# Kernel optimization log

Measured on AMD Instinct MI355X. Metric: run time of the kernel, lower is better.

The kernel has to match this reference:

```python
import jax, jax.numpy as jnp
import numpy as np
import math

D_MODEL = 1024
N_HEADS = 16
D_K = D_MODEL // N_HEADS
MAX_REL = 32


def setup_inputs() -> dict:
    key = jax.random.key(0)
    ks = jax.random.split(key, 8)
    B, S = 8, 1024
    x = jax.random.normal(ks[0], (B, S, D_MODEL), dtype=jnp.float32)
    scale = 1.0 / math.sqrt(D_MODEL)
    Wq = jax.random.normal(ks[1], (D_MODEL, D_MODEL), dtype=jnp.float32) * scale
    Wk = jax.random.normal(ks[2], (D_MODEL, D_MODEL), dtype=jnp.float32) * scale
    Wv = jax.random.normal(ks[3], (D_MODEL, D_MODEL), dtype=jnp.float32) * scale
    Wo = jax.random.normal(ks[4], (D_MODEL, D_MODEL), dtype=jnp.float32) * scale
    b_o = jnp.zeros((D_MODEL,), dtype=jnp.float32)
    rel_k_emb = jax.random.normal(ks[5], (2 * MAX_REL + 1, D_K), dtype=jnp.float32) * 0.02
    rel_v_emb = jax.random.normal(ks[6], (2 * MAX_REL + 1, D_K), dtype=jnp.float32) * 0.02
    return {"x": x, "Wq": Wq, "Wk": Wk, "Wv": Wv, "Wo": Wo, "b_o": b_o,
            "rel_k_emb": rel_k_emb, "rel_v_emb": rel_v_emb}


def reference(x, Wq, Wk, Wv, Wo, b_o, rel_k_emb, rel_v_emb):
    B, S, D = x.shape
    H, dk = N_HEADS, D_K
    inv_sqrt_dk = 1.0 / math.sqrt(dk)
    # projections (torch Linear: x @ W.T), split heads -> [B, S, H, dk]
    Q = (x @ Wq.T).reshape(B, S, H, dk)
    K = (x @ Wk.T).reshape(B, S, H, dk)
    V = (x @ Wv.T).reshape(B, S, H, dk)
    # relative position indices: clip(j - i, -M, M) + M  -> [S, S]
    pos = jnp.arange(S)
    rel_idx = jnp.clip(pos[None, :] - pos[:, None], -MAX_REL, MAX_REL) + MAX_REL
    rel_k = rel_k_emb[rel_idx]  # [S, S, dk]
    rel_v = rel_v_emb[rel_idx]  # [S, S, dk]
    # scores: content term + Shaw relative-key term, both scaled by 1/sqrt(dk)
    scores = jnp.einsum('bihd,bjhd->bhij', Q, K) * inv_sqrt_dk
    scores = scores + jnp.einsum('bihd,ijd->bhij', Q, rel_k) * inv_sqrt_dk
    attn = jax.nn.softmax(scores, axis=-1)  # [B, H, S, S]
    # context: attn @ V + Shaw relative-value term
    ctx = jnp.einsum('bhij,bjhd->bihd', attn, V)
    ctx = ctx + jnp.einsum('bhij,ijd->bihd', attn, rel_v)
    ctx = ctx.reshape(B, S, D)
    out = ctx @ Wo.T + b_o
    return out
```

## Files before the change

### kernel.cpp

```cpp
#include <hip/hip_runtime.h>
#include <hip/hip_bf16.h>
#include <stdint.h>

typedef __bf16 bf16;
typedef __bf16 bf16x8 __attribute__((ext_vector_type(8)));
typedef short s16x4 __attribute__((ext_vector_type(4)));
typedef float f32x4 __attribute__((ext_vector_type(4)));

#define DEVI __device__ __forceinline__

static constexpr int QREL_ST = 80;
static constexpr float SCL2 = 0.1803368801111244f;

DEVI void gload_lds16(const void* g, void* l) {
  __builtin_amdgcn_global_load_lds(
      (const __attribute__((address_space(1))) void*)g,
      (__attribute__((address_space(3))) void*)l, 16, 0, 0);
}

__global__ __launch_bounds__(256) void k_cvt(const float* __restrict__ s,
                                             bf16* __restrict__ d, int n4) {
  int i = blockIdx.x * 256 + threadIdx.x;
  if (i >= n4) return;
  float4 v = ((const float4*)s)[i];
  union { bf16 b[4]; ushort4 u; } pk;
  pk.b[0] = (bf16)v.x; pk.b[1] = (bf16)v.y;
  pk.b[2] = (bf16)v.z; pk.b[3] = (bf16)v.w;
  ((ushort4*)d)[i] = pk.u;
}

__global__ __launch_bounds__(256) void k_cvtw(const float* __restrict__ a,
                                              const float* __restrict__ b,
                                              const float* __restrict__ c,
                                              const float* __restrict__ e,
                                              bf16* __restrict__ d) {
  int z = blockIdx.y;
  const float* s = (z == 0) ? a : (z == 1) ? b : (z == 2) ? c : e;
  int i = blockIdx.x * 256 + threadIdx.x;
  float4 v = ((const float4*)s)[i];
  union { bf16 bb[4]; ushort4 u; } pk;
  pk.bb[0] = (bf16)v.x; pk.bb[1] = (bf16)v.y;
  pk.bb[2] = (bf16)v.z; pk.bb[3] = (bf16)v.w;
  ((ushort4*)(d + (size_t)z * 1048576))[i] = pk.u;
}

template <int MODE>
DEVI void gemm_core(const bf16* __restrict__ A, const bf16* __restrict__ W,
                    const float* __restrict__ bo, bf16* __restrict__ OutB,
                    float* __restrict__ OutF, int m0, int n0) {
  const int tid = threadIdx.x, wid = tid >> 6, lane = tid & 63;
  const int wr = wid >> 1, wc = wid & 1;
  __shared__ __attribute__((aligned(16))) bf16 As[128 * 32];
  __shared__ __attribute__((aligned(16))) bf16 Bs[128 * 32];
  f32x4 acc[4][4] = {};
  const int lrow = lane >> 2, lcol = (lane & 3) * 8;
  for (int k0 = 0; k0 < 1024; k0 += 32) {
    for (int c = wid; c < 8; c += 4) {
      gload_lds16(&A[(size_t)(m0 + c * 16 + lrow) * 1024 + k0 + lcol], &As[c * 512]);
      gload_lds16(&W[(size_t)(n0 + c * 16 + lrow) * 1024 + k0 + lcol], &Bs[c * 512]);
    }
    __syncthreads();
    bf16x8 af[4], bw[4];
#pragma unroll
    for (int f = 0; f < 4; ++f) {
      af[f] = *(const bf16x8*)&As[(wr * 64 + f * 16 + (lane & 15)) * 32 + (lane >> 4) * 8];
      bw[f] = *(const bf16x8*)&Bs[(wc * 64 + f * 16 + (lane & 15)) * 32 + (lane >> 4) * 8];
    }
#pragma unroll
    for (int fm = 0; fm < 4; ++fm)
#pragma unroll
      for (int fn = 0; fn < 4; ++fn)
        acc[fm][fn] = __builtin_amdgcn_mfma_f32_16x16x32_bf16(af[fm], bw[fn], acc[fm][fn], 0, 0, 0);
    __syncthreads();
  }
#pragma unroll
  for (int fm = 0; fm < 4; ++fm)
#pragma unroll
    for (int fn = 0; fn < 4; ++fn)
#pragma unroll
      for (int r = 0; r < 4; ++r) {
        int m = m0 + wr * 64 + fm * 16 + (lane >> 4) * 4 + r;
        int n = n0 + wc * 64 + fn * 16 + (lane & 15);
        if (MODE == 0) {
          size_t o = ((size_t)((m >> 10) * 16 + (n >> 6)) * 1024 + (m & 1023)) * 64 + (n & 63);
          OutB[o] = (bf16)acc[fm][fn][r];
        } else {
          OutF[(size_t)m * 1024 + n] = acc[fm][fn][r] + bo[n];
        }
      }
}

__global__ __launch_bounds__(256) void k_gemm_qkv(const bf16* __restrict__ A,
                                                  const bf16* __restrict__ Wb,
                                                  bf16* __restrict__ Qb,
                                                  bf16* __restrict__ Kb,
                                                  bf16* __restrict__ Vb) {
  const int z = blockIdx.z;
  const bf16* W = Wb + (size_t)z * 1024 * 1024;
  bf16* Out = (z == 0) ? Qb : ((z == 1) ? Kb : Vb);
  gemm_core<0>(A, W, nullptr, Out, nullptr, blockIdx.x * 128, blockIdx.y * 128);
}

__global__ __launch_bounds__(256) void k_gemm_out(const bf16* __restrict__ A,
                                                  const bf16* __restrict__ W,
                                                  const float* __restrict__ bo,
                                                  float* __restrict__ Out) {
  gemm_core<1>(A, W, bo, nullptr, Out, blockIdx.x * 128, blockIdx.y * 128);
}

__global__ __launch_bounds__(256) void k_transpose(const bf16* __restrict__ Vb,
                                                   bf16* __restrict__ Vt) {
  const int s0 = blockIdx.x * 64, bh = blockIdx.y;
  __shared__ __attribute__((aligned(16))) bf16 T[64 * 72];
  const int tid = threadIdx.x;
#pragma unroll
  for (int c = 0; c < 2; ++c) {
    int flat = c * 256 + tid;
    int row = flat >> 3, c8 = (flat & 7) * 8;
    *(uint4*)&T[row * 72 + c8] =
        *(const uint4*)&Vb[((size_t)bh * 1024 + s0 + row) * 64 + c8];
  }
  __syncthreads();
  const int d = tid >> 2, j0 = (tid & 3) * 16;
  union { bf16 b[16]; uint4 u[2]; } pk;
#pragma unroll
  for (int j = 0; j < 16; ++j) pk.b[j] = T[(j0 + j) * 72 + d];
  size_t base = ((size_t)bh * 64 + d) * 1024 + s0 + j0;
  *(uint4*)&Vt[base] = pk.u[0];
  *(uint4*)&Vt[base + 8] = pk.u[1];
}

__global__ __launch_bounds__(256) void k_qrel(const bf16* __restrict__ Qb,
                                              const float* __restrict__ relk,
                                              bf16* __restrict__ Qrel) {
  const int m0 = blockIdx.x * 64;
  const int tid = threadIdx.x, wid = tid >> 6, lane = tid & 63;
  __shared__ __attribute__((aligned(16))) bf16 RK[80 * 72];
  for (int i = tid; i < 80 * 72; i += 256) {
    int r = i / 72, dd = i % 72;
    RK[i] = (r < 65 && dd < 64) ? (bf16)relk[r * 64 + dd] : (bf16)0.0f;
  }
  __syncthreads();
  bf16x8 qa[2];
#pragma unroll
  for (int kk = 0; kk < 2; ++kk)
    qa[kk] = *(const bf16x8*)&Qb[(size_t)(m0 + wid * 16 + (lane & 15)) * 64 + kk * 32 + (lane >> 4) * 8];
  f32x4 acc[5] = {};
#pragma unroll
  for (int fc = 0; fc < 5; ++fc)
#pragma unroll
    for (int kk = 0; kk < 2; ++kk) {
      bf16x8 rb = *(const bf16x8*)&RK[(fc * 16 + (lane & 15)) * 72 + kk * 32 + (lane >> 4) * 8];
      acc[fc] = __builtin_amdgcn_mfma_f32_16x16x32_bf16(qa[kk], rb, acc[fc], 0, 0, 0);
    }
#pragma unroll
  for (int fc = 0; fc < 5; ++fc)
#pragma unroll
    for (int r = 0; r < 4; ++r)
      Qrel[(size_t)(m0 + wid * 16 + (lane >> 4) * 4 + r) * QREL_ST + fc * 16 + (lane & 15)] =
          (bf16)(acc[fc][r] * SCL2);
}

__global__ __launch_bounds__(256) void k_prep(const float* __restrict__ relv,
                                              bf16* __restrict__ RVt) {
  int i = blockIdx.x * 256 + threadIdx.x;
  if (i >= 64 * 96) return;
  int d = i / 96, r = i % 96;
  RVt[i] = (r < 65) ? (bf16)relv[r * 64 + d] : (bf16)0.0f;
}

__global__ __launch_bounds__(256, 4) void k_attn(const bf16* __restrict__ Qb,
                                                 const bf16* __restrict__ Kb,
                                                 const bf16* __restrict__ Vt,
                                                 const bf16* __restrict__ Qrel,
                                                 const bf16* __restrict__ RVt,
                                                 const float* __restrict__ relv,
                                                 bf16* __restrict__ Ctx) {
  const int jb = blockIdx.x;
  const int xcd = jb & 7, rlin = jb >> 3;
  const int bh = xcd + 8 * (rlin >> 4);
  const int tq = rlin & 15, q0 = tq * 64;
  const int tid = threadIdx.x, wid = tid >> 6, lane = tid & 63;
  __shared__ __attribute__((aligned(16))) bf16 Qrl[64 * 72];
  __shared__ __attribute__((aligned(16))) bf16 KS[64 * 64];
  __shared__ __attribute__((aligned(16))) bf16 VS[64 * 64];
  __shared__ __attribute__((aligned(16))) bf16 BUK[64 * 64];

  for (int i = tid; i < 576; i += 256) {
    int row = i / 9, u4 = (i % 9) * 8;
    *(uint4*)&Qrl[row * 72 + u4] =
        *(const uint4*)&Qrel[((size_t)bh * 1024 + q0 + row) * QREL_ST + u4];
  }
  {
    uint4 z4 = {0, 0, 0, 0};
    uint4* bz = (uint4*)BUK;
    for (int i = tid; i < 512; i += 256) bz[i] = z4;
  }

  const int q16 = lane & 15, lhi = lane >> 4;
  const int qrow = wid * 16 + q16;
  const int qglob = q0 + qrow;
  const size_t kvb = (size_t)bh * 65536;

  const int srow = lane >> 3;
  const int scol = (((lane & 7) ^ srow)) * 8;

  const bf16* kg0 = Kb + kvb + (size_t)((wid * 2 + 0) * 8 + srow) * 64 + scol;
  const bf16* kg1 = Kb + kvb + (size_t)((wid * 2 + 1) * 8 + srow) * 64 + scol;
  const bf16* vg0 = Vt + kvb + (size_t)((wid * 2 + 0) * 8 + srow) * 1024 + scol;
  const bf16* vg1 = Vt + kvb + (size_t)((wid * 2 + 1) * 8 + srow) * 1024 + scol;
  bf16* kd0 = &KS[(wid * 2 + 0) * 512];
  bf16* kd1 = &KS[(wid * 2 + 1) * 512];
  bf16* vd0 = &VS[(wid * 2 + 0) * 512];
  bf16* vd1 = &VS[(wid * 2 + 1) * 512];

#define STAGE_ISSUE()                                                          \
  do {                                                                         \
    gload_lds16(kg0, kd0); gload_lds16(kg1, kd1);                              \
    gload_lds16(vg0, vd0); gload_lds16(vg1, vd1);                              \
    kg0 += 4096; kg1 += 4096; vg0 += 64; vg1 += 64;                            \
  } while (0)

  bf16x8 qa[2];
#pragma unroll
  for (int kk = 0; kk < 2; ++kk)
    qa[kk] = *(const bf16x8*)&Qb[kvb + (size_t)qglob * 64 + kk * 32 + lhi * 8];

  f32x4 o[4] = {};
  float rowsum = 0.f, sumL = 0.f, sumR = 0.f;

  union PU { bf16 b[4]; s16x4 s; };
  union VU { uint2 u; s16x4 s; };

  STAGE_ISSUE();
  __syncthreads();
  const float biasL = (float)Qrl[qrow * 72 + 0];
  const float biasR = (float)Qrl[qrow * 72 + 64];

  const int swz = (q16 & 7) * 8;
  const bf16* kp0 = &KS[q16 * 64 + ((lhi * 8) ^ swz)];
  const bf16* kp1 = &KS[q16 * 64 + ((32 + lhi * 8) ^ swz)];
  const bf16* vp[4] = {
      &VS[q16 * 64 + ((0 * 16 + lhi * 4) ^ swz)],
      &VS[q16 * 64 + ((1 * 16 + lhi * 4) ^ swz)],
      &VS[q16 * 64 + ((2 * 16 + lhi * 4) ^ swz)],
      &VS[q16 * 64 + ((3 * 16 + lhi * 4) ^ swz)]};
  const bf16* qrp = &Qrl[qrow * 72 + 32];
  bf16* bkp = &BUK[qrow * 64 + 32];

  for (int t = 0; t < 16; ++t) {
    const int kv0 = t * 64;
    const int kind = (t <= tq - 2) ? 0 : (t >= tq + 2) ? 1 : 2;
    f32x4 st[4] = {};
    __builtin_amdgcn_s_setprio(1);
#pragma unroll
    for (int jt = 0; jt < 4; ++jt) {
      bf16x8 k0 = *(const bf16x8*)(kp0 + jt * 1024);
      bf16x8 k1 = *(const bf16x8*)(kp1 + jt * 1024);
      st[jt] = __builtin_amdgcn_mfma_f32_16x16x32_bf16(k0, qa[0], st[jt], 0, 0, 0);
      st[jt] = __builtin_amdgcn_mfma_f32_16x16x32_bf16(k1, qa[1], st[jt], 0, 0, 0);
    }
    __builtin_amdgcn_s_setprio(0);
    PU pk[4];
    if (kind == 0) {
#pragma unroll
      for (int jt = 0; jt < 4; ++jt)
#pragma unroll
        for (int r = 0; r < 4; ++r) {
          float p = __builtin_amdgcn_exp2f(__builtin_fmaf(st[jt][r], SCL2, biasL));
          rowsum += p; sumL += p;
          pk[jt].b[r] = (bf16)p;
        }
    } else if (kind == 1) {
#pragma unroll
      for (int jt = 0; jt < 4; ++jt)
#pragma unroll
        for (int r = 0; r < 4; ++r) {
          float p = __builtin_amdgcn_exp2f(__builtin_fmaf(st[jt][r], SCL2, biasR));
          rowsum += p; sumR += p;
          pk[jt].b[r] = (bf16)p;
        }
    } else {
#pragma unroll
      for (int jt = 0; jt < 4; ++jt)
#pragma unroll
        for (int r = 0; r < 4; ++r) {
          const int j = kv0 + jt * 16 + lhi * 4 + r;
          const int delta = j - qglob;
          const int dc = delta < -32 ? -32 : (delta > 32 ? 32 : delta);
          const float b = (float)qrp[dc];
          float p = __builtin_amdgcn_exp2f(__builtin_fmaf(st[jt][r], SCL2, b));
          rowsum += p;
          pk[jt].b[r] = (bf16)p;
          if (delta <= -32) sumL += p;
          else if (delta >= 32) sumR += p;
          else bkp[delta] = (bf16)p;
        }
    }
    __builtin_amdgcn_s_setprio(1);
#pragma unroll
    for (int jt = 0; jt < 4; ++jt)
#pragma unroll
      for (int fd = 0; fd < 4; ++fd) {
        VU v;
        v.u = *(const uint2*)(vp[jt] + fd * 1024);
        o[fd] = __builtin_amdgcn_mfma_f32_16x16x16bf16_1k(pk[jt].s, v.s, o[fd], 0, 0, 0);
      }
    __builtin_amdgcn_s_setprio(0);
    __syncthreads();
    if (t < 15) {
      STAGE_ISSUE();
      __syncthreads();
    }
  }
#undef STAGE_ISSUE

  rowsum += __shfl_xor(rowsum, 16, 64);
  rowsum += __shfl_xor(rowsum, 32, 64);
  sumL += __shfl_xor(sumL, 16, 64);
  sumL += __shfl_xor(sumL, 32, 64);
  sumR += __shfl_xor(sumR, 16, 64);
  sumR += __shfl_xor(sumR, 32, 64);
  if (lhi == 0) BUK[qrow * 64 + 0] = (bf16)sumL;

  float linv[4], sumRr[4];
#pragma unroll
  for (int r = 0; r < 4; ++r) {
    linv[r] = 1.0f / __shfl(rowsum, lhi * 4 + r, 16);
    sumRr[r] = __shfl(sumR, lhi * 4 + r, 16);
  }

#pragma unroll
  for (int kk = 0; kk < 2; ++kk) {
    bf16x8 pa = *(const bf16x8*)&BUK[(wid * 16 + q16) * 64 + kk * 32 + lhi * 8];
#pragma unroll
    for (int fd = 0; fd < 4; ++fd) {
      bf16x8 rb = *(const bf16x8*)&RVt[(fd * 16 + q16) * 96 + kk * 32 + lhi * 8];
      o[fd] = __builtin_amdgcn_mfma_f32_16x16x32_bf16(pa, rb, o[fd], 0, 0, 0);
    }
  }
#pragma unroll
  for (int fd = 0; fd < 4; ++fd) {
    float rv64 = relv[64 * 64 + fd * 16 + q16];
#pragma unroll
    for (int r = 0; r < 4; ++r) o[fd][r] += sumRr[r] * rv64;
  }

  const int rbase = wid * 16 + lhi * 4;
  __syncthreads();
  bf16* OL = Qrl;
#pragma unroll
  for (int fd = 0; fd < 4; ++fd)
#pragma unroll
    for (int r = 0; r < 4; ++r)
      OL[(rbase + r) * 72 + fd * 16 + q16] = (bf16)(o[fd][r] * linv[r]);
  __syncthreads();
  {
    int il = tid >> 2, d0 = (tid & 3) * 16;
    union { bf16 b[16]; uint4 u[2]; } pkk;
#pragma unroll
    for (int c = 0; c < 16; ++c) pkk.b[c] = OL[il * 72 + d0 + c];
    size_t base = ((size_t)(bh >> 4) * 1024 + q0 + il) * 1024 + (bh & 15) * 64 + d0;
    *(uint4*)&Ctx[base] = pkk.u[0];
    *(uint4*)&Ctx[base + 8] = pkk.u[1];
  }
}

extern "C" void kernel_launch(void* const* d_in, const int* in_sizes, int n_in,
                              void* d_out, int out_size, void* d_ws, size_t ws_size,
                              hipStream_t stream) {
  const float* x = (const float*)d_in[0];
  const float* Wq = (const float*)d_in[1];
  const float* Wk = (const float*)d_in[2];
  const float* Wv = (const float*)d_in[3];
  const float* Wo = (const float*)d_in[4];
  const float* bo = (const float*)d_in[5];
  const float* relk = (const float*)d_in[6];
  const float* relv = (const float*)d_in[7];
  float* out = (float*)d_out;

  uint8_t* w = (uint8_t*)d_ws;
  bf16* xb = (bf16*)(w);
  bf16* Wb = (bf16*)(w + 16777216);
  bf16* Qb = (bf16*)(w + 25165824);
  bf16* Kb = (bf16*)(w + 41943040);
  bf16* Vb = (bf16*)(w + 58720256);
  bf16* Vt = (bf16*)(w + 75497472);
  bf16* Qrel = (bf16*)(w + 92274688);
  bf16* Ctx = Vb;
  bf16* RVt = xb;

  k_cvt<<<8192, 256, 0, stream>>>(x, xb, 2097152);
  k_cvtw<<<dim3(1024, 4), 256, 0, stream>>>(Wq, Wk, Wv, Wo, Wb);

  dim3 gg(64, 8, 3);
  k_gemm_qkv<<<gg, 256, 0, stream>>>(xb, Wb, Qb, Kb, Vb);
  k_transpose<<<dim3(16, 128), 256, 0, stream>>>(Vb, Vt);
  k_qrel<<<2048, 256, 0, stream>>>(Qb, relk, Qrel);
  k_prep<<<24, 256, 0, stream>>>(relv, RVt);
  k_attn<<<2048, 256, 0, stream>>>(Qb, Kb, Vt, Qrel, RVt, relv, Ctx);
  k_gemm_out<<<dim3(64, 8), 256, 0, stream>>>(Ctx, Wb + 3 * 1048576, bo, out);
}
```

Before: 199.7 us.

## Double-buffer K/V tiles in attention and XCD-remap GEMM block indices

The attention kernel now keeps two K/V LDS buffers and prefetches tile t+2 while computing tile t. It waits with explicit vmcnt counts and raw barriers instead of two syncthreads per iteration, which is meant to hide global-to-LDS latency. The LDS footprint grows, so occupancy is lowered to 3 blocks. The QKV and output GEMMs switch to a 1D grid whose block index is remapped so neighbouring tiles land on the same XCD, aiming at better L2 reuse.

```diff
diff --git a/kernel.cpp b/kernel.cpp
--- a/kernel.cpp
+++ b/kernel.cpp
@@ -95,17 +95,22 @@
                                                   bf16* __restrict__ Qb,
                                                   bf16* __restrict__ Kb,
                                                   bf16* __restrict__ Vb) {
-  const int z = blockIdx.z;
+  const int j = blockIdx.x;
+  const int l = (j & 7) * 192 + (j >> 3);
+  const int x = l & 63, y = (l >> 6) & 7, z = l >> 9;
   const bf16* W = Wb + (size_t)z * 1024 * 1024;
   bf16* Out = (z == 0) ? Qb : ((z == 1) ? Kb : Vb);
-  gemm_core<0>(A, W, nullptr, Out, nullptr, blockIdx.x * 128, blockIdx.y * 128);
+  gemm_core<0>(A, W, nullptr, Out, nullptr, x * 128, y * 128);
 }
 
 __global__ __launch_bounds__(256) void k_gemm_out(const bf16* __restrict__ A,
                                                   const bf16* __restrict__ W,
                                                   const float* __restrict__ bo,
                                                   float* __restrict__ Out) {
-  gemm_core<1>(A, W, bo, nullptr, Out, blockIdx.x * 128, blockIdx.y * 128);
+  const int j = blockIdx.x;
+  const int l = (j & 7) * 64 + (j >> 3);
+  const int x = l & 63, y = l >> 6;
+  gemm_core<1>(A, W, bo, nullptr, Out, x * 128, y * 128);
 }
 
 __global__ __launch_bounds__(256) void k_transpose(const bf16* __restrict__ Vb,
@@ -169,7 +174,7 @@
   RVt[i] = (r < 65) ? (bf16)relv[r * 64 + d] : (bf16)0.0f;
 }
 
-__global__ __launch_bounds__(256, 4) void k_attn(const bf16* __restrict__ Qb,
+__global__ __launch_bounds__(256, 3) void k_attn(const bf16* __restrict__ Qb,
                                                  const bf16* __restrict__ Kb,
                                                  const bf16* __restrict__ Vt,
                                                  const bf16* __restrict__ Qrel,
@@ -182,8 +187,8 @@
   const int tq = rlin & 15, q0 = tq * 64;
   const int tid = threadIdx.x, wid = tid >> 6, lane = tid & 63;
   __shared__ __attribute__((aligned(16))) bf16 Qrl[64 * 72];
-  __shared__ __attribute__((aligned(16))) bf16 KS[64 * 64];
-  __shared__ __attribute__((aligned(16))) bf16 VS[64 * 64];
+  __shared__ __attribute__((aligned(16))) bf16 KS[2 * 64 * 64];
+  __shared__ __attribute__((aligned(16))) bf16 VS[2 * 64 * 64];
   __shared__ __attribute__((aligned(16))) bf16 BUK[64 * 64];
 
   for (int i = tid; i < 576; i += 256) {
@@ -209,15 +214,13 @@
   const bf16* kg1 = Kb + kvb + (size_t)((wid * 2 + 1) * 8 + srow) * 64 + scol;
   const bf16* vg0 = Vt + kvb + (size_t)((wid * 2 + 0) * 8 + srow) * 1024 + scol;
   const bf16* vg1 = Vt + kvb + (size_t)((wid * 2 + 1) * 8 + srow) * 1024 + scol;
-  bf16* kd0 = &KS[(wid * 2 + 0) * 512];
-  bf16* kd1 = &KS[(wid * 2 + 1) * 512];
-  bf16* vd0 = &VS[(wid * 2 + 0) * 512];
-  bf16* vd1 = &VS[(wid * 2 + 1) * 512];
-
-#define STAGE_ISSUE()                                                          \
+  const int c0 = (wid * 2 + 0) * 512, c1 = (wid * 2 + 1) * 512;
+
+#define STAGE(T)                                                               \
   do {                                                                         \
-    gload_lds16(kg0, kd0); gload_lds16(kg1, kd1);                              \
-    gload_lds16(vg0, vd0); gload_lds16(vg1, vd1);                              \
+    const int b_ = ((T) & 1) * 4096;                                           \
+    gload_lds16(kg0, &KS[b_ + c0]); gload_lds16(kg1, &KS[b_ + c1]);            \
+    gload_lds16(vg0, &VS[b_ + c0]); gload_lds16(vg1, &VS[b_ + c1]);            \
     kg0 += 4096; kg1 += 4096; vg0 += 64; vg1 += 64;                            \
   } while (0)
 
@@ -232,7 +235,8 @@
   union PU { bf16 b[4]; s16x4 s; };
   union VU { uint2 u; s16x4 s; };
 
-  STAGE_ISSUE();
+  STAGE(0);
+  STAGE(1);
   __syncthreads();
   const float biasL = (float)Qrl[qrow * 72 + 0];
   const float biasR = (float)Qrl[qrow * 72 + 64];
@@ -249,14 +253,20 @@
   bf16* bkp = &BUK[qrow * 64 + 32];
 
   for (int t = 0; t < 16; ++t) {
+    if (t < 15) asm volatile("s_waitcnt vmcnt(4)" ::: "memory");
+    else        asm volatile("s_waitcnt vmcnt(0)" ::: "memory");
+    __builtin_amdgcn_s_barrier();
+    __builtin_amdgcn_sched_barrier(0);
+
     const int kv0 = t * 64;
+    const int boff = (t & 1) * 4096;
     const int kind = (t <= tq - 2) ? 0 : (t >= tq + 2) ? 1 : 2;
     f32x4 st[4] = {};
     __builtin_amdgcn_s_setprio(1);
 #pragma unroll
     for (int jt = 0; jt < 4; ++jt) {
-      bf16x8 k0 = *(const bf16x8*)(kp0 + jt * 1024);
-      bf16x8 k1 = *(const bf16x8*)(kp1 + jt * 1024);
+      bf16x8 k0 = *(const bf16x8*)(kp0 + boff + jt * 1024);
+      bf16x8 k1 = *(const bf16x8*)(kp1 + boff + jt * 1024);
       st[jt] = __builtin_amdgcn_mfma_f32_16x16x32_bf16(k0, qa[0], st[jt], 0, 0, 0);
       st[jt] = __builtin_amdgcn_mfma_f32_16x16x32_bf16(k1, qa[1], st[jt], 0, 0, 0);
     }
@@ -303,17 +313,15 @@
 #pragma unroll
       for (int fd = 0; fd < 4; ++fd) {
         VU v;
-        v.u = *(const uint2*)(vp[jt] + fd * 1024);
+        v.u = *(const uint2*)(vp[jt] + boff + fd * 1024);
         o[fd] = __builtin_amdgcn_mfma_f32_16x16x16bf16_1k(pk[jt].s, v.s, o[fd], 0, 0, 0);
       }
     __builtin_amdgcn_s_setprio(0);
-    __syncthreads();
-    if (t < 15) {
-      STAGE_ISSUE();
-      __syncthreads();
-    }
-  }
-#undef STAGE_ISSUE
+
+    __builtin_amdgcn_s_barrier();
+    if (t < 14) STAGE(t + 2);
+  }
+#undef STAGE
 
   rowsum += __shfl_xor(rowsum, 16, 64);
   rowsum += __shfl_xor(rowsum, 32, 64);
@@ -393,11 +401,10 @@
   k_cvt<<<8192, 256, 0, stream>>>(x, xb, 2097152);
   k_cvtw<<<dim3(1024, 4), 256, 0, stream>>>(Wq, Wk, Wv, Wo, Wb);
 
-  dim3 gg(64, 8, 3);
-  k_gemm_qkv<<<gg, 256, 0, stream>>>(xb, Wb, Qb, Kb, Vb);
+  k_gemm_qkv<<<1536, 256, 0, stream>>>(xb, Wb, Qb, Kb, Vb);
   k_transpose<<<dim3(16, 128), 256, 0, stream>>>(Vb, Vt);
   k_qrel<<<2048, 256, 0, stream>>>(Qb, relk, Qrel);
   k_prep<<<24, 256, 0, stream>>>(relv, RVt);
   k_attn<<<2048, 256, 0, stream>>>(Qb, Kb, Vt, Qrel, RVt, relv, Ctx);
-  k_gemm_out<<<dim3(64, 8), 256, 0, stream>>>(Ctx, Wb + 3 * 1048576, bo, out);
-}
+  k_gemm_out<<<512, 256, 0, stream>>>(Ctx, Wb + 3 * 1048576, bo, out);
+}
```

Result: slower. 220.4 us (+10.3%).

## Enlarge attention query tile to 128 rows with 512-thread blocks

Applied to the files above, without the earlier changes.

The attention kernel now handles 128 query rows per block with 8 waves instead of 64 rows with 4 waves, so each K/V tile loaded into LDS serves twice as many queries. Each wave issues half as many staged loads, and the near/far classification of each tile is now done per wave rather than per block. The cost is more LDS per block (larger Qrel and bucket buffers), half as many blocks, and a 512-thread barrier on every iteration, which may reduce occupancy and latency hiding.

```diff
diff --git a/kernel.cpp b/kernel.cpp
--- a/kernel.cpp
+++ b/kernel.cpp
@@ -169,7 +169,7 @@
   RVt[i] = (r < 65) ? (bf16)relv[r * 64 + d] : (bf16)0.0f;
 }
 
-__global__ __launch_bounds__(256, 4) void k_attn(const bf16* __restrict__ Qb,
+__global__ __launch_bounds__(512, 6) void k_attn(const bf16* __restrict__ Qb,
                                                  const bf16* __restrict__ Kb,
                                                  const bf16* __restrict__ Vt,
                                                  const bf16* __restrict__ Qrel,
@@ -178,15 +178,15 @@
                                                  bf16* __restrict__ Ctx) {
   const int jb = blockIdx.x;
   const int xcd = jb & 7, rlin = jb >> 3;
-  const int bh = xcd + 8 * (rlin >> 4);
-  const int tq = rlin & 15, q0 = tq * 64;
+  const int bh = xcd + 8 * (rlin >> 3);
+  const int q0 = (rlin & 7) * 128;
   const int tid = threadIdx.x, wid = tid >> 6, lane = tid & 63;
-  __shared__ __attribute__((aligned(16))) bf16 Qrl[64 * 72];
+  __shared__ __attribute__((aligned(16))) bf16 Qrl[128 * 72];
   __shared__ __attribute__((aligned(16))) bf16 KS[64 * 64];
   __shared__ __attribute__((aligned(16))) bf16 VS[64 * 64];
-  __shared__ __attribute__((aligned(16))) bf16 BUK[64 * 64];
-
-  for (int i = tid; i < 576; i += 256) {
+  __shared__ __attribute__((aligned(16))) bf16 BUK[128 * 64];
+
+  for (int i = tid; i < 1152; i += 512) {
     int row = i / 9, u4 = (i % 9) * 8;
     *(uint4*)&Qrl[row * 72 + u4] =
         *(const uint4*)&Qrel[((size_t)bh * 1024 + q0 + row) * QREL_ST + u4];
@@ -194,31 +194,26 @@
   {
     uint4 z4 = {0, 0, 0, 0};
     uint4* bz = (uint4*)BUK;
-    for (int i = tid; i < 512; i += 256) bz[i] = z4;
+    for (int i = tid; i < 1024; i += 512) bz[i] = z4;
   }
 
   const int q16 = lane & 15, lhi = lane >> 4;
   const int qrow = wid * 16 + q16;
   const int qglob = q0 + qrow;
+  const int wq = q0 + wid * 16;
   const size_t kvb = (size_t)bh * 65536;
 
   const int srow = lane >> 3;
-  const int scol = (((lane & 7) ^ srow)) * 8;
-
-  const bf16* kg0 = Kb + kvb + (size_t)((wid * 2 + 0) * 8 + srow) * 64 + scol;
-  const bf16* kg1 = Kb + kvb + (size_t)((wid * 2 + 1) * 8 + srow) * 64 + scol;
-  const bf16* vg0 = Vt + kvb + (size_t)((wid * 2 + 0) * 8 + srow) * 1024 + scol;
-  const bf16* vg1 = Vt + kvb + (size_t)((wid * 2 + 1) * 8 + srow) * 1024 + scol;
-  bf16* kd0 = &KS[(wid * 2 + 0) * 512];
-  bf16* kd1 = &KS[(wid * 2 + 1) * 512];
-  bf16* vd0 = &VS[(wid * 2 + 0) * 512];
-  bf16* vd1 = &VS[(wid * 2 + 1) * 512];
-
-#define STAGE_ISSUE()                                                          \
+  const int scol = ((lane & 7) ^ srow) * 8;
+  const bf16* kg = Kb + kvb + (size_t)(wid * 8 + srow) * 64 + scol;
+  const bf16* vg = Vt + kvb + (size_t)(wid * 8 + srow) * 1024 + scol;
+  bf16* kd = &KS[wid * 512];
+  bf16* vd = &VS[wid * 512];
+
+#define STAGE()                                                                \
   do {                                                                         \
-    gload_lds16(kg0, kd0); gload_lds16(kg1, kd1);                              \
-    gload_lds16(vg0, vd0); gload_lds16(vg1, vd1);                              \
-    kg0 += 4096; kg1 += 4096; vg0 += 64; vg1 += 64;                            \
+    gload_lds16(kg, kd); gload_lds16(vg, vd);                                  \
+    kg += 4096; vg += 64;                                                      \
   } while (0)
 
   bf16x8 qa[2];
@@ -232,7 +227,7 @@
   union PU { bf16 b[4]; s16x4 s; };
   union VU { uint2 u; s16x4 s; };
 
-  STAGE_ISSUE();
+  STAGE();
   __syncthreads();
   const float biasL = (float)Qrl[qrow * 72 + 0];
   const float biasR = (float)Qrl[qrow * 72 + 64];
@@ -250,7 +245,7 @@
 
   for (int t = 0; t < 16; ++t) {
     const int kv0 = t * 64;
-    const int kind = (t <= tq - 2) ? 0 : (t >= tq + 2) ? 1 : 2;
+    const int kind = (kv0 + 95 <= wq) ? 0 : (kv0 >= wq + 47) ? 1 : 2;
     f32x4 st[4] = {};
     __builtin_amdgcn_s_setprio(1);
 #pragma unroll
@@ -309,11 +304,11 @@
     __builtin_amdgcn_s_setprio(0);
     __syncthreads();
     if (t < 15) {
-      STAGE_ISSUE();
+      STAGE();
       __syncthreads();
     }
   }
-#undef STAGE_ISSUE
+#undef STAGE
 
   rowsum += __shfl_xor(rowsum, 16, 64);
   rowsum += __shfl_xor(rowsum, 32, 64);
@@ -398,6 +393,6 @@
   k_transpose<<<dim3(16, 128), 256, 0, stream>>>(Vb, Vt);
   k_qrel<<<2048, 256, 0, stream>>>(Qb, relk, Qrel);
   k_prep<<<24, 256, 0, stream>>>(relv, RVt);
-  k_attn<<<2048, 256, 0, stream>>>(Qb, Kb, Vt, Qrel, RVt, relv, Ctx);
+  k_attn<<<1024, 512, 0, stream>>>(Qb, Kb, Vt, Qrel, RVt, relv, Ctx);
   k_gemm_out<<<dim3(64, 8), 256, 0, stream>>>(Ctx, Wb + 3 * 1048576, bo, out);
 }
```

Measured after the change: 203.3 us. No clear change (+1.8%).

## Process 128 query rows per attention block to reuse K/V tiles

Applied to the files above, without the earlier changes.

Each attention block now covers 128 query rows instead of 64, and each wave handles two 16-row query tiles that share the same K and V fragments read from LDS. The goal is to halve global K/V staging traffic and LDS reads per query, and to halve the number of blocks launched. In exchange, register and LDS use per block grow, occupancy drops (launch bounds go from 4 to 3 blocks), and the grid shrinks to 1024 blocks. The per-tile region classification is rewritten per 16-row subtile using query offsets.

```diff
diff --git a/kernel.cpp b/kernel.cpp
--- a/kernel.cpp
+++ b/kernel.cpp
@@ -169,7 +169,7 @@
   RVt[i] = (r < 65) ? (bf16)relv[r * 64 + d] : (bf16)0.0f;
 }
 
-__global__ __launch_bounds__(256, 4) void k_attn(const bf16* __restrict__ Qb,
+__global__ __launch_bounds__(256, 3) void k_attn(const bf16* __restrict__ Qb,
                                                  const bf16* __restrict__ Kb,
                                                  const bf16* __restrict__ Vt,
                                                  const bf16* __restrict__ Qrel,
@@ -178,15 +178,15 @@
                                                  bf16* __restrict__ Ctx) {
   const int jb = blockIdx.x;
   const int xcd = jb & 7, rlin = jb >> 3;
-  const int bh = xcd + 8 * (rlin >> 4);
-  const int tq = rlin & 15, q0 = tq * 64;
+  const int bh = xcd + 8 * (rlin >> 3);
+  const int q0 = (rlin & 7) * 128;
   const int tid = threadIdx.x, wid = tid >> 6, lane = tid & 63;
-  __shared__ __attribute__((aligned(16))) bf16 Qrl[64 * 72];
+  __shared__ __attribute__((aligned(16))) bf16 Qrl[128 * 72];
   __shared__ __attribute__((aligned(16))) bf16 KS[64 * 64];
   __shared__ __attribute__((aligned(16))) bf16 VS[64 * 64];
-  __shared__ __attribute__((aligned(16))) bf16 BUK[64 * 64];
-
-  for (int i = tid; i < 576; i += 256) {
+  __shared__ __attribute__((aligned(16))) bf16 BUK[128 * 64];
+
+  for (int i = tid; i < 1152; i += 256) {
     int row = i / 9, u4 = (i % 9) * 8;
     *(uint4*)&Qrl[row * 72 + u4] =
         *(const uint4*)&Qrel[((size_t)bh * 1024 + q0 + row) * QREL_ST + u4];
@@ -194,17 +194,18 @@
   {
     uint4 z4 = {0, 0, 0, 0};
     uint4* bz = (uint4*)BUK;
-    for (int i = tid; i < 512; i += 256) bz[i] = z4;
+    for (int i = tid; i < 1024; i += 256) bz[i] = z4;
   }
 
   const int q16 = lane & 15, lhi = lane >> 4;
-  const int qrow = wid * 16 + q16;
-  const int qglob = q0 + qrow;
+  const int qrowA = wid * 32 + q16;
+  const int qrowB = qrowA + 16;
+  const int qglobA = q0 + qrowA, qglobB = q0 + qrowB;
+  const int wqA = q0 + wid * 32, wqB = wqA + 16;
   const size_t kvb = (size_t)bh * 65536;
 
   const int srow = lane >> 3;
   const int scol = (((lane & 7) ^ srow)) * 8;
-
   const bf16* kg0 = Kb + kvb + (size_t)((wid * 2 + 0) * 8 + srow) * 64 + scol;
   const bf16* kg1 = Kb + kvb + (size_t)((wid * 2 + 1) * 8 + srow) * 64 + scol;
   const bf16* vg0 = Vt + kvb + (size_t)((wid * 2 + 0) * 8 + srow) * 1024 + scol;
@@ -214,28 +215,33 @@
   bf16* vd0 = &VS[(wid * 2 + 0) * 512];
   bf16* vd1 = &VS[(wid * 2 + 1) * 512];
 
-#define STAGE_ISSUE()                                                          \
+#define STAGE()                                                                \
   do {                                                                         \
     gload_lds16(kg0, kd0); gload_lds16(kg1, kd1);                              \
     gload_lds16(vg0, vd0); gload_lds16(vg1, vd1);                              \
     kg0 += 4096; kg1 += 4096; vg0 += 64; vg1 += 64;                            \
   } while (0)
 
-  bf16x8 qa[2];
-#pragma unroll
-  for (int kk = 0; kk < 2; ++kk)
-    qa[kk] = *(const bf16x8*)&Qb[kvb + (size_t)qglob * 64 + kk * 32 + lhi * 8];
-
-  f32x4 o[4] = {};
-  float rowsum = 0.f, sumL = 0.f, sumR = 0.f;
+  bf16x8 qaA[2], qaB[2];
+#pragma unroll
+  for (int kk = 0; kk < 2; ++kk) {
+    qaA[kk] = *(const bf16x8*)&Qb[kvb + (size_t)qglobA * 64 + kk * 32 + lhi * 8];
+    qaB[kk] = *(const bf16x8*)&Qb[kvb + (size_t)qglobB * 64 + kk * 32 + lhi * 8];
+  }
+
+  f32x4 oA[4] = {}, oB[4] = {};
+  float rsA = 0.f, slA = 0.f, srA = 0.f;
+  float rsB = 0.f, slB = 0.f, srB = 0.f;
 
   union PU { bf16 b[4]; s16x4 s; };
   union VU { uint2 u; s16x4 s; };
 
-  STAGE_ISSUE();
+  STAGE();
   __syncthreads();
-  const float biasL = (float)Qrl[qrow * 72 + 0];
-  const float biasR = (float)Qrl[qrow * 72 + 64];
+  const float biasLA = (float)Qrl[qrowA * 72 + 0];
+  const float biasRA = (float)Qrl[qrowA * 72 + 64];
+  const float biasLB = (float)Qrl[qrowB * 72 + 0];
+  const float biasRB = (float)Qrl[qrowB * 72 + 64];
 
   const int swz = (q16 & 7) * 8;
   const bf16* kp0 = &KS[q16 * 64 + ((lhi * 8) ^ swz)];
@@ -245,58 +251,60 @@
       &VS[q16 * 64 + ((1 * 16 + lhi * 4) ^ swz)],
       &VS[q16 * 64 + ((2 * 16 + lhi * 4) ^ swz)],
       &VS[q16 * 64 + ((3 * 16 + lhi * 4) ^ swz)]};
-  const bf16* qrp = &Qrl[qrow * 72 + 32];
-  bf16* bkp = &BUK[qrow * 64 + 32];
+  const bf16* qrpA = &Qrl[qrowA * 72 + 32];
+  const bf16* qrpB = &Qrl[qrowB * 72 + 32];
+  bf16* bkpA = &BUK[qrowA * 64 + 32];
+  bf16* bkpB = &BUK[qrowB * 64 + 32];
+
+#define EXP_SET(ST, PK, BL, BR, QG, QRPp, BKPp, RS, SL, SR, KIND)              \
+  do {                                                                         \
+    if ((KIND) == 0) {                                                         \
+      _Pragma("unroll") for (int jt = 0; jt < 4; ++jt)                         \
+      _Pragma("unroll") for (int r = 0; r < 4; ++r) {                          \
+        float p = __builtin_amdgcn_exp2f(__builtin_fmaf((ST)[jt][r], SCL2, (BL))); \
+        (RS) += p; (SL) += p; (PK)[jt].b[r] = (bf16)p;                         \
+      }                                                                        \
+    } else if ((KIND) == 1) {                                                  \
+      _Pragma("unroll") for (int jt = 0; jt < 4; ++jt)                         \
+      _Pragma("unroll") for (int r = 0; r < 4; ++r) {                          \
+        float p = __builtin_amdgcn_exp2f(__builtin_fmaf((ST)[jt][r], SCL2, (BR))); \
+        (RS) += p; (SR) += p; (PK)[jt].b[r] = (bf16)p;                         \
+      }                                                                        \
+    } else {                                                                   \
+      _Pragma("unroll") for (int jt = 0; jt < 4; ++jt)                         \
+      _Pragma("unroll") for (int r = 0; r < 4; ++r) {                          \
+        const int j = kv0 + jt * 16 + lhi * 4 + r;                             \
+        const int delta = j - (QG);                                            \
+        const int dc = delta < -32 ? -32 : (delta > 32 ? 32 : delta);          \
+        const float b = (float)(QRPp)[dc];                                     \
+        float p = __builtin_amdgcn_exp2f(__builtin_fmaf((ST)[jt][r], SCL2, b));\
+        (RS) += p; (PK)[jt].b[r] = (bf16)p;                                    \
+        if (delta <= -32) (SL) += p;                                           \
+        else if (delta >= 32) (SR) += p;                                       \
+        else (BKPp)[delta] = (bf16)p;                                          \
+      }                                                                        \
+    }                                                                          \
+  } while (0)
 
   for (int t = 0; t < 16; ++t) {
     const int kv0 = t * 64;
-    const int kind = (t <= tq - 2) ? 0 : (t >= tq + 2) ? 1 : 2;
-    f32x4 st[4] = {};
+    const int kindA = (kv0 + 95 <= wqA) ? 0 : (kv0 >= wqA + 47) ? 1 : 2;
+    const int kindB = (kv0 + 95 <= wqB) ? 0 : (kv0 >= wqB + 47) ? 1 : 2;
+    f32x4 stA[4] = {}, stB[4] = {};
     __builtin_amdgcn_s_setprio(1);
 #pragma unroll
     for (int jt = 0; jt < 4; ++jt) {
       bf16x8 k0 = *(const bf16x8*)(kp0 + jt * 1024);
       bf16x8 k1 = *(const bf16x8*)(kp1 + jt * 1024);
-      st[jt] = __builtin_amdgcn_mfma_f32_16x16x32_bf16(k0, qa[0], st[jt], 0, 0, 0);
-      st[jt] = __builtin_amdgcn_mfma_f32_16x16x32_bf16(k1, qa[1], st[jt], 0, 0, 0);
+      stA[jt] = __builtin_amdgcn_mfma_f32_16x16x32_bf16(k0, qaA[0], stA[jt], 0, 0, 0);
+      stA[jt] = __builtin_amdgcn_mfma_f32_16x16x32_bf16(k1, qaA[1], stA[jt], 0, 0, 0);
+      stB[jt] = __builtin_amdgcn_mfma_f32_16x16x32_bf16(k0, qaB[0], stB[jt], 0, 0, 0);
+      stB[jt] = __builtin_amdgcn_mfma_f32_16x16x32_bf16(k1, qaB[1], stB[jt], 0, 0, 0);
     }
     __builtin_amdgcn_s_setprio(0);
-    PU pk[4];
-    if (kind == 0) {
-#pragma unroll
-      for (int jt = 0; jt < 4; ++jt)
-#pragma unroll
-        for (int r = 0; r < 4; ++r) {
-          float p = __builtin_amdgcn_exp2f(__builtin_fmaf(st[jt][r], SCL2, biasL));
-          rowsum += p; sumL += p;
-          pk[jt].b[r] = (bf16)p;
-        }
-    } else if (kind == 1) {
-#pragma unroll
-      for (int jt = 0; jt < 4; ++jt)
-#pragma unroll
-        for (int r = 0; r < 4; ++r) {
-          float p = __builtin_amdgcn_exp2f(__builtin_fmaf(st[jt][r], SCL2, biasR));
-          rowsum += p; sumR += p;
-          pk[jt].b[r] = (bf16)p;
-        }
-    } else {
-#pragma unroll
-      for (int jt = 0; jt < 4; ++jt)
-#pragma unroll
-        for (int r = 0; r < 4; ++r) {
-          const int j = kv0 + jt * 16 + lhi * 4 + r;
-          const int delta = j - qglob;
-          const int dc = delta < -32 ? -32 : (delta > 32 ? 32 : delta);
-          const float b = (float)qrp[dc];
-          float p = __builtin_amdgcn_exp2f(__builtin_fmaf(st[jt][r], SCL2, b));
-          rowsum += p;
-          pk[jt].b[r] = (bf16)p;
-          if (delta <= -32) sumL += p;
-          else if (delta >= 32) sumR += p;
-          else bkp[delta] = (bf16)p;
-        }
-    }
+    PU pkA[4], pkB[4];
+    EXP_SET(stA, pkA, biasLA, biasRA, qglobA, qrpA, bkpA, rsA, slA, srA, kindA);
+    EXP_SET(stB, pkB, biasLB, biasRB, qglobB, qrpB, bkpB, rsB, slB, srB, kindB);
     __builtin_amdgcn_s_setprio(1);
 #pragma unroll
     for (int jt = 0; jt < 4; ++jt)
@@ -304,65 +312,82 @@
       for (int fd = 0; fd < 4; ++fd) {
         VU v;
         v.u = *(const uint2*)(vp[jt] + fd * 1024);
-        o[fd] = __builtin_amdgcn_mfma_f32_16x16x16bf16_1k(pk[jt].s, v.s, o[fd], 0, 0, 0);
+        oA[fd] = __builtin_amdgcn_mfma_f32_16x16x16bf16_1k(pkA[jt].s, v.s, oA[fd], 0, 0, 0);
+        oB[fd] = __builtin_amdgcn_mfma_f32_16x16x16bf16_1k(pkB[jt].s, v.s, oB[fd], 0, 0, 0);
       }
     __builtin_amdgcn_s_setprio(0);
     __syncthreads();
     if (t < 15) {
-      STAGE_ISSUE();
+      STAGE();
       __syncthreads();
     }
   }
-#undef STAGE_ISSUE
-
-  rowsum += __shfl_xor(rowsum, 16, 64);
-  rowsum += __shfl_xor(rowsum, 32, 64);
-  sumL += __shfl_xor(sumL, 16, 64);
-  sumL += __shfl_xor(sumL, 32, 64);
-  sumR += __shfl_xor(sumR, 16, 64);
-  sumR += __shfl_xor(sumR, 32, 64);
-  if (lhi == 0) BUK[qrow * 64 + 0] = (bf16)sumL;
-
-  float linv[4], sumRr[4];
+#undef STAGE
+#undef EXP_SET
+
+  rsA += __shfl_xor(rsA, 16, 64); rsA += __shfl_xor(rsA, 32, 64);
+  slA += __shfl_xor(slA, 16, 64); slA += __shfl_xor(slA, 32, 64);
+  srA += __shfl_xor(srA, 16, 64); srA += __shfl_xor(srA, 32, 64);
+  rsB += __shfl_xor(rsB, 16, 64); rsB += __shfl_xor(rsB, 32, 64);
+  slB += __shfl_xor(slB, 16, 64); slB += __shfl_xor(slB, 32, 64);
+  srB += __shfl_xor(srB, 16, 64); srB += __shfl_xor(srB, 32, 64);
+  if (lhi == 0) {
+    BUK[qrowA * 64 + 0] = (bf16)slA;
+    BUK[qrowB * 64 + 0] = (bf16)slB;
+  }
+
+  float linvA[4], srrA[4], linvB[4], srrB[4];
 #pragma unroll
   for (int r = 0; r < 4; ++r) {
-    linv[r] = 1.0f / __shfl(rowsum, lhi * 4 + r, 16);
-    sumRr[r] = __shfl(sumR, lhi * 4 + r, 16);
+    linvA[r] = 1.0f / __shfl(rsA, lhi * 4 + r, 16);
+    srrA[r] = __shfl(srA, lhi * 4 + r, 16);
+    linvB[r] = 1.0f / __shfl(rsB, lhi * 4 + r, 16);
+    srrB[r] = __shfl(srB, lhi * 4 + r, 16);
   }
 
 #pragma unroll
   for (int kk = 0; kk < 2; ++kk) {
-    bf16x8 pa = *(const bf16x8*)&BUK[(wid * 16 + q16) * 64 + kk * 32 + lhi * 8];
+    bf16x8 paA = *(const bf16x8*)&BUK[(wid * 32 + q16) * 64 + kk * 32 + lhi * 8];
+    bf16x8 paB = *(const bf16x8*)&BUK[(wid * 32 + 16 + q16) * 64 + kk * 32 + lhi * 8];
 #pragma unroll
     for (int fd = 0; fd < 4; ++fd) {
       bf16x8 rb = *(const bf16x8*)&RVt[(fd * 16 + q16) * 96 + kk * 32 + lhi * 8];
-      o[fd] = __builtin_amdgcn_mfma_f32_16x16x32_bf16(pa, rb, o[fd], 0, 0, 0);
+      oA[fd] = __builtin_amdgcn_mfma_f32_16x16x32_bf16(paA, rb, oA[fd], 0, 0, 0);
+      oB[fd] = __builtin_amdgcn_mfma_f32_16x16x32_bf16(paB, rb, oB[fd], 0, 0, 0);
     }
   }
 #pragma unroll
   for (int fd = 0; fd < 4; ++fd) {
     float rv64 = relv[64 * 64 + fd * 16 + q16];
 #pragma unroll
-    for (int r = 0; r < 4; ++r) o[fd][r] += sumRr[r] * rv64;
-  }
-
-  const int rbase = wid * 16 + lhi * 4;
+    for (int r = 0; r < 4; ++r) {
+      oA[fd][r] += srrA[r] * rv64;
+      oB[fd][r] += srrB[r] * rv64;
+    }
+  }
+
+  const int rbaseA = wid * 32 + lhi * 4, rbaseB = rbaseA + 16;
   __syncthreads();
   bf16* OL = Qrl;
 #pragma unroll
   for (int fd = 0; fd < 4; ++fd)
 #pragma unroll
-    for (int r = 0; r < 4; ++r)
-      OL[(rbase + r) * 72 + fd * 16 + q16] = (bf16)(o[fd][r] * linv[r]);
+    for (int r = 0; r < 4; ++r) {
+      OL[(rbaseA + r) * 72 + fd * 16 + q16] = (bf16)(oA[fd][r] * linvA[r]);
+      OL[(rbaseB + r) * 72 + fd * 16 + q16] = (bf16)(oB[fd][r] * linvB[r]);
+    }
   __syncthreads();
   {
-    int il = tid >> 2, d0 = (tid & 3) * 16;
-    union { bf16 b[16]; uint4 u[2]; } pkk;
-#pragma unroll
-    for (int c = 0; c < 16; ++c) pkk.b[c] = OL[il * 72 + d0 + c];
-    size_t base = ((size_t)(bh >> 4) * 1024 + q0 + il) * 1024 + (bh & 15) * 64 + d0;
-    *(uint4*)&Ctx[base] = pkk.u[0];
-    *(uint4*)&Ctx[base + 8] = pkk.u[1];
+#pragma unroll
+    for (int half = 0; half < 2; ++half) {
+      int il = half * 64 + (tid >> 2), d0 = (tid & 3) * 16;
+      union { bf16 b[16]; uint4 u[2]; } pkk;
+#pragma unroll
+      for (int c = 0; c < 16; ++c) pkk.b[c] = OL[il * 72 + d0 + c];
+      size_t base = ((size_t)(bh >> 4) * 1024 + q0 + il) * 1024 + (bh & 15) * 64 + d0;
+      *(uint4*)&Ctx[base] = pkk.u[0];
+      *(uint4*)&Ctx[base + 8] = pkk.u[1];
+    }
   }
 }
 
@@ -398,6 +423,6 @@
   k_transpose<<<dim3(16, 128), 256, 0, stream>>>(Vb, Vt);
   k_qrel<<<2048, 256, 0, stream>>>(Qb, relk, Qrel);
   k_prep<<<24, 256, 0, stream>>>(relv, RVt);
-  k_attn<<<2048, 256, 0, stream>>>(Qb, Kb, Vt, Qrel, RVt, relv, Ctx);
+  k_attn<<<1024, 256, 0, stream>>>(Qb, Kb, Vt, Qrel, RVt, relv, Ctx);
   k_gemm_out<<<dim3(64, 8), 256, 0, stream>>>(Ctx, Wb + 3 * 1048576, bo, out);
 }
```

New measurement: 207.0 us. 3.6% more time.
